# Kernel tuning notes

Hardware: AMD Instinct MI355X
Metric: run time of the kernel (lower is better)

## Reference

```python
import jax, jax.numpy as jnp
import numpy as np

BS, V, C, A = 8, 4096, 64, 12   # batch, vertices, channels, anchors (anchor_size=12 hardcoded in source)
K = 4                            # neighbor_num
POOLING_RATE = 4
POOL = V // POOLING_RATE


def setup_inputs() -> dict:
    key = jax.random.key(0)
    k1, k2, k3 = jax.random.split(key, 3)
    vertices = jax.random.normal(k1, (BS, V, 3), dtype=jnp.float32)
    feature_map = jax.random.normal(k2, (BS, C, V, A), dtype=jnp.float32)
    # deterministic stand-in for torch.randperm(V)[:POOL]
    sample_idx = jax.random.permutation(k3, V)[:POOL].astype(jnp.int32)
    return {"vertices": vertices, "feature_map": feature_map, "sample_idx": sample_idx}


def reference(vertices, feature_map, sample_idx):
    bs, v, _ = vertices.shape
    c, a = feature_map.shape[1], feature_map.shape[3]
    k = K
    # pairwise squared euclidean distances: (bs, v, v)
    inner = jnp.einsum('bic,bjc->bij', vertices, vertices)
    quad = jnp.sum(vertices * vertices, axis=2)                     # (bs, v)
    dist = -2.0 * inner + quad[:, None, :] + quad[:, :, None]
    # k+1 smallest, drop self (first entry)
    _, idx = jax.lax.top_k(-dist, k + 1)                            # (bs, v, k+1)
    nbr = idx[:, :, 1:]                                             # (bs, v, k)
    # gather neighbor features along vertex axis (axis=2 of feature_map)
    idx_b = jnp.broadcast_to(nbr.reshape(bs, 1, v * k, 1), (bs, c, v * k, a))
    nbr_feat = jnp.take_along_axis(feature_map, idx_b, axis=2)      # (bs, c, v*k, a)
    nbr_feat = nbr_feat.reshape(bs, c, v, k, a)
    pooled = jnp.max(nbr_feat, axis=3)                              # (bs, c, v, a)
    vertices_pool = vertices[:, sample_idx, :]                      # (bs, pool, 3)
    feature_map_pool = pooled[:, :, sample_idx, :]                  # (bs, c, pool, a)
    return vertices_pool, feature_map_pool
```

## Files before the change

### kernel.cpp

```cpp
#include <hip/hip_runtime.h>
#include <stdint.h>

#define BS 8
#define V 4096
#define C 64
#define A 12
#define POOL 1024

__device__ inline unsigned int ordu(float f) {
    unsigned int b = __float_as_uint(f);
    return b ^ ((unsigned int)(((int)b) >> 31) | 0x80000000u);
}
__device__ inline float unordu(unsigned int u) {
    unsigned int m = (~((unsigned int)(((int)u) >> 31))) | 0x80000000u;
    return __uint_as_float(u ^ m);
}

template<int NCC>
__global__ __launch_bounds__(256) void knn_chunk_kernel(
    const float* __restrict__ vtx,
    const int* __restrict__ sidx,
    unsigned long long* __restrict__ partial,
    unsigned int* __restrict__ counts)
{
    constexpr int CC = V / NCC;
    __shared__ float4 cand[CC];

    const int bid = blockIdx.x;
    const int tid = threadIdx.x;
    if (bid < (BS * V) / 256) counts[bid * 256 + tid] = 0;

    const int cc = bid % NCC;
    const int qc = (bid / NCC) & 3;
    const int b  = bid / (NCC * 4);

    const float* vb = vtx + (size_t)b * V * 3;

    for (int t = tid; t < CC; t += 256) {
        const int j = cc * CC + t;
        const float x = vb[j * 3 + 0];
        const float y = vb[j * 3 + 1];
        const float z = vb[j * 3 + 2];
        float q;
        {
#pragma clang fp contract(off)
            q = (x * x + y * y) + z * z;
        }
        cand[t] = make_float4(x, y, z, q);
    }
    __syncthreads();

    const int s = qc * 256 + tid;
    const int gq = sidx[s];
    const float qx = vb[gq * 3 + 0];
    const float qy = vb[gq * 3 + 1];
    const float qz = vb[gq * 3 + 2];
    float qq;
    {
#pragma clang fp contract(off)
        qq = (qx * qx + qy * qy) + qz * qz;
    }

    unsigned int h0 = ~0u, h1 = ~0u, h2 = ~0u, h3 = ~0u, h4 = ~0u;
    unsigned int l0 = 0, l1 = 0, l2 = 0, l3 = 0, l4 = 0;

#pragma unroll 8
    for (int jj = 0; jj < CC; ++jj) {
        const float4 cd = cand[jj];
        const float inner = fmaf(cd.z, qz, fmaf(cd.y, qy, cd.x * qx));
        const float d = fmaf(-2.0f, inner, cd.w) + qq;
        const unsigned int bits = __float_as_uint(d);
        const unsigned int u = bits ^ ((unsigned int)(((int)bits) >> 31) | 0x80000000u);
        const unsigned int idx = (unsigned int)(cc * CC + jj);
        if (u < h4) {
            const bool c0 = u < h0, c1 = u < h1, c2 = u < h2, c3 = u < h3;
            h4 = c3 ? h3 : u;              l4 = c3 ? l3 : idx;
            h3 = c3 ? (c2 ? h2 : u) : h3;  l3 = c3 ? (c2 ? l2 : idx) : l3;
            h2 = c2 ? (c1 ? h1 : u) : h2;  l2 = c2 ? (c1 ? l1 : idx) : l2;
            h1 = c1 ? (c0 ? h0 : u) : h1;  l1 = c1 ? (c0 ? l0 : idx) : l1;
            h0 = c0 ? u : h0;              l0 = c0 ? idx : l0;
        }
    }

    unsigned long long* p = partial + ((size_t)(b * POOL + s) * NCC + cc) * 5;
    p[0] = ((unsigned long long)h0 << 32) | l0;
    p[1] = ((unsigned long long)h1 << 32) | l1;
    p[2] = ((unsigned long long)h2 << 32) | l2;
    p[3] = ((unsigned long long)h3 << 32) | l3;
    p[4] = ((unsigned long long)h4 << 32) | l4;
}

template<int NCC>
__global__ __launch_bounds__(256) void knn_merge_kernel(
    const unsigned long long* __restrict__ partial,
    const float* __restrict__ vtx,
    const int* __restrict__ sidx,
    int* __restrict__ nbr,
    float* __restrict__ outv,
    unsigned int* __restrict__ counts)
{
    const int t = blockIdx.x * 256 + threadIdx.x;
    const int b = t / POOL;
    const int s = t % POOL;

    const unsigned long long* p = partial + (size_t)t * (NCC * 5);

    unsigned int h0 = ~0u, h1 = ~0u, h2 = ~0u, h3 = ~0u, h4 = ~0u;
    unsigned int l0 = 0, l1 = 0, l2 = 0, l3 = 0, l4 = 0;

#pragma unroll 4
    for (int ccc = 0; ccc < NCC; ++ccc) {
        const unsigned long long a0 = p[ccc * 5 + 0];
        const unsigned long long a1 = p[ccc * 5 + 1];
        const unsigned long long a2 = p[ccc * 5 + 2];
        const unsigned long long a3 = p[ccc * 5 + 3];
        const unsigned long long a4 = p[ccc * 5 + 4];
        if ((unsigned int)(a0 >> 32) < h4) {
#define INS(K)                                                               \
            {                                                                \
                const unsigned int u = (unsigned int)((K) >> 32);            \
                const unsigned int idx = (unsigned int)(K);                  \
                const bool c0 = u < h0, c1 = u < h1, c2 = u < h2,            \
                           c3 = u < h3, c4 = u < h4;                         \
                h4 = c4 ? (c3 ? h3 : u) : h4;                                \
                l4 = c4 ? (c3 ? l3 : idx) : l4;                              \
                h3 = c3 ? (c2 ? h2 : u) : h3;                                \
                l3 = c3 ? (c2 ? l2 : idx) : l3;                              \
                h2 = c2 ? (c1 ? h1 : u) : h2;                                \
                l2 = c2 ? (c1 ? l1 : idx) : l2;                              \
                h1 = c1 ? (c0 ? h0 : u) : h1;                                \
                l1 = c1 ? (c0 ? l0 : idx) : l1;                              \
                h0 = c0 ? u : h0;                                            \
                l0 = c0 ? idx : l0;                                          \
            }
            INS(a0) INS(a1) INS(a2) INS(a3) INS(a4)
#undef INS
        }
    }

    int4 nb;
    nb.x = (int)l1;
    nb.y = (int)l2;
    nb.z = (int)l3;
    nb.w = (int)l4;
    ((int4*)nbr)[t] = nb;

    unsigned int* cb = counts + b * V;
    atomicAdd(&cb[l1], 1u);
    atomicAdd(&cb[l2], 1u);
    atomicAdd(&cb[l3], 1u);
    atomicAdd(&cb[l4], 1u);

    const int gq = sidx[s];
    const float* vv = vtx + ((size_t)b * V + gq) * 3;
    outv[(size_t)t * 3 + 0] = vv[0];
    outv[(size_t)t * 3 + 1] = vv[1];
    outv[(size_t)t * 3 + 2] = vv[2];
}

__global__ __launch_bounds__(256) void scan_kernel(
    const unsigned int* __restrict__ counts,
    unsigned int* __restrict__ rowptr,
    unsigned int* __restrict__ cursors)
{
    const int b = blockIdx.x;
    const int tid = threadIdx.x;
    __shared__ unsigned int psum[256];

    const unsigned int* cb = counts + b * V;
    unsigned int local[16];
    unsigned int sum = 0;
#pragma unroll
    for (int i = 0; i < 16; ++i) { local[i] = sum; sum += cb[tid * 16 + i]; }
    psum[tid] = sum;
    __syncthreads();

    for (int off = 1; off < 256; off <<= 1) {
        unsigned int v = (tid >= off) ? psum[tid - off] : 0u;
        __syncthreads();
        psum[tid] += v;
        __syncthreads();
    }
    const unsigned int base = (tid == 0) ? 0u : psum[tid - 1];

    unsigned int* rp = rowptr + b * (V + 1);
    unsigned int* cu = cursors + b * V;
#pragma unroll
    for (int i = 0; i < 16; ++i) {
        const unsigned int e = base + local[i];
        rp[tid * 16 + i] = e;
        cu[tid * 16 + i] = e;
    }
    if (tid == 255) rp[V] = base + sum;
}

__global__ __launch_bounds__(256) void fill_kernel(
    const int* __restrict__ nbr,
    unsigned int* __restrict__ cursors,
    unsigned int* __restrict__ entries)
{
    const int t = blockIdx.x * 256 + threadIdx.x;
    const int b = t / POOL;
    const unsigned int s = (unsigned int)(t % POOL);
    const int4 nb = ((const int4*)nbr)[t];
    unsigned int* cu = cursors + b * V;
    unsigned int* en = entries + b * 4096;
    en[atomicAdd(&cu[nb.x], 1u)] = s;
    en[atomicAdd(&cu[nb.y], 1u)] = s;
    en[atomicAdd(&cu[nb.z], 1u)] = s;
    en[atomicAdd(&cu[nb.w], 1u)] = s;
}

__global__ __launch_bounds__(512) void pool_kernel(
    const float* __restrict__ fm,
    const unsigned int* __restrict__ rowptr,
    const unsigned int* __restrict__ entries,
    float* __restrict__ outf)
{
    __shared__ unsigned int pl[POOL * A];
    const int c = blockIdx.x % C;
    const int b = blockIdx.x / C;
    const int tid = threadIdx.x;

    {
        uint4* p4 = (uint4*)pl;
        const uint4 z = make_uint4(0u, 0u, 0u, 0u);
#pragma unroll
        for (int i = 0; i < 6; ++i) p4[tid + i * 512] = z;
    }
    __syncthreads();

    const unsigned int* rp = rowptr + b * (V + 1);
    const unsigned int* en = entries + b * 4096;
    const float4* plane = (const float4*)(fm + (size_t)(b * C + c) * V * A);

#pragma unroll 1
    for (int it = 0; it < V / 512; ++it) {
        const int j = it * 512 + tid;
        const unsigned int beg = rp[j];
        const unsigned int end = rp[j + 1];
        if (beg == end) continue;

        const float4 f0 = plane[j * 3 + 0];
        const float4 f1 = plane[j * 3 + 1];
        const float4 f2 = plane[j * 3 + 2];
        const unsigned int u0 = ordu(f0.x), u1 = ordu(f0.y), u2  = ordu(f0.z), u3  = ordu(f0.w);
        const unsigned int u4 = ordu(f1.x), u5 = ordu(f1.y), u6  = ordu(f1.z), u7  = ordu(f1.w);
        const unsigned int u8 = ordu(f2.x), u9 = ordu(f2.y), u10 = ordu(f2.z), u11 = ordu(f2.w);

        for (unsigned int e = beg; e < end; ++e) {
            unsigned int* d = pl + en[e] * A;
            atomicMax(d + 0, u0);  atomicMax(d + 1, u1);  atomicMax(d + 2, u2);
            atomicMax(d + 3, u3);  atomicMax(d + 4, u4);  atomicMax(d + 5, u5);
            atomicMax(d + 6, u6);  atomicMax(d + 7, u7);  atomicMax(d + 8, u8);
            atomicMax(d + 9, u9);  atomicMax(d + 10, u10); atomicMax(d + 11, u11);
        }
    }
    __syncthreads();

    const uint4* p4 = (const uint4*)pl;
    float4* dst = (float4*)(outf + (size_t)(b * C + c) * POOL * A);
#pragma unroll
    for (int i = 0; i < 6; ++i) {
        const uint4 v = p4[tid + i * 512];
        float4 f;
        f.x = unordu(v.x); f.y = unordu(v.y); f.z = unordu(v.z); f.w = unordu(v.w);
        dst[tid + i * 512] = f;
    }
}

extern "C" void kernel_launch(void* const* d_in, const int* in_sizes, int n_in,
                              void* d_out, int out_size, void* d_ws, size_t ws_size,
                              hipStream_t stream) {
    const float* vtx = (const float*)d_in[0];
    const float* fm  = (const float*)d_in[1];
    const int* sidx  = (const int*)d_in[2];
    float* out = (float*)d_out;

    float* outv = out;
    float* outf = out + (size_t)BS * POOL * 3;

    char* ws = (char*)d_ws;
    const size_t partial32_b = (size_t)BS * POOL * 32 * 5 * 8;
    const size_t partial16_b = (size_t)BS * POOL * 16 * 5 * 8;
    const size_t nbr_b     = (size_t)BS * POOL * 4 * 4;
    const size_t counts_b  = (size_t)BS * V * 4;
    const size_t rowptr_b  = (size_t)BS * (V + 1) * 4 + 28;
    const size_t cursors_b = (size_t)BS * V * 4;
    const size_t entries_b = (size_t)BS * 4096 * 4;
    const size_t tail_b = nbr_b + counts_b + rowptr_b + cursors_b + entries_b;

    const bool big = ws_size >= partial32_b + tail_b;
    const size_t partial_b = big ? partial32_b : partial16_b;

    unsigned long long* partial = (unsigned long long*)ws;
    int* nbr            = (int*)(ws + partial_b);
    unsigned int* counts  = (unsigned int*)(ws + partial_b + nbr_b);
    unsigned int* rowptr  = (unsigned int*)(ws + partial_b + nbr_b + counts_b);
    unsigned int* cursors = (unsigned int*)(ws + partial_b + nbr_b + counts_b + rowptr_b);
    unsigned int* entries = (unsigned int*)(ws + partial_b + nbr_b + counts_b + rowptr_b + cursors_b);

    if (big) {
        constexpr int NCC = 32;
        knn_chunk_kernel<NCC><<<BS * 4 * NCC, 256, 0, stream>>>(vtx, sidx, partial, counts);
        knn_merge_kernel<NCC><<<(BS * POOL) / 256, 256, 0, stream>>>(partial, vtx, sidx, nbr, outv, counts);
    } else {
        constexpr int NCC = 16;
        knn_chunk_kernel<NCC><<<BS * 4 * NCC, 256, 0, stream>>>(vtx, sidx, partial, counts);
        knn_merge_kernel<NCC><<<(BS * POOL) / 256, 256, 0, stream>>>(partial, vtx, sidx, nbr, outv, counts);
    }
    scan_kernel<<<BS, 256, 0, stream>>>(counts, rowptr, cursors);
    fill_kernel<<<(BS * POOL) / 256, 256, 0, stream>>>(nbr, cursors, entries);
    pool_kernel<<<BS * C, 512, 0, stream>>>(fm, rowptr, entries, outf);
}
```

Before: 229.1 us.

## Fuse scan and fill kernels, pad pooling LDS stride, compare floats in kNN

Merges the scan and fill kernels into one per-batch kernel that keeps the cursors in shared memory, which removes a launch and the global cursor array with its global atomics. The pool kernel pads each pooled row to a stride of 13 words in LDS to cut bank conflicts on the atomicMax scatter and the readback, at the cost of scalar LDS reads and more shared memory. The kNN chunk loop now compares float distances directly and converts them to ordered uints only at the final store. Fill parallelism drops to 8 blocks, and the LDS use per pool block grows.

```diff
diff --git a/kernel.cpp b/kernel.cpp
--- a/kernel.cpp
+++ b/kernel.cpp
@@ -6,6 +6,7 @@
 #define C 64
 #define A 12
 #define POOL 1024
+#define PSTRIDE 13
 
 __device__ inline unsigned int ordu(float f) {
     unsigned int b = __float_as_uint(f);
@@ -61,7 +62,8 @@
         qq = (qx * qx + qy * qy) + qz * qz;
     }
 
-    unsigned int h0 = ~0u, h1 = ~0u, h2 = ~0u, h3 = ~0u, h4 = ~0u;
+    const float INF = __uint_as_float(0x7F800000u);
+    float d0 = INF, d1 = INF, d2 = INF, d3 = INF, d4 = INF;
     unsigned int l0 = 0, l1 = 0, l2 = 0, l3 = 0, l4 = 0;
 
 #pragma unroll 8
@@ -69,25 +71,23 @@
         const float4 cd = cand[jj];
         const float inner = fmaf(cd.z, qz, fmaf(cd.y, qy, cd.x * qx));
         const float d = fmaf(-2.0f, inner, cd.w) + qq;
-        const unsigned int bits = __float_as_uint(d);
-        const unsigned int u = bits ^ ((unsigned int)(((int)bits) >> 31) | 0x80000000u);
         const unsigned int idx = (unsigned int)(cc * CC + jj);
-        if (u < h4) {
-            const bool c0 = u < h0, c1 = u < h1, c2 = u < h2, c3 = u < h3;
-            h4 = c3 ? h3 : u;              l4 = c3 ? l3 : idx;
-            h3 = c3 ? (c2 ? h2 : u) : h3;  l3 = c3 ? (c2 ? l2 : idx) : l3;
-            h2 = c2 ? (c1 ? h1 : u) : h2;  l2 = c2 ? (c1 ? l1 : idx) : l2;
-            h1 = c1 ? (c0 ? h0 : u) : h1;  l1 = c1 ? (c0 ? l0 : idx) : l1;
-            h0 = c0 ? u : h0;              l0 = c0 ? idx : l0;
+        if (d < d4) {
+            const bool c0 = d < d0, c1 = d < d1, c2 = d < d2, c3 = d < d3;
+            d4 = c3 ? d3 : d;              l4 = c3 ? l3 : idx;
+            d3 = c3 ? (c2 ? d2 : d) : d3;  l3 = c3 ? (c2 ? l2 : idx) : l3;
+            d2 = c2 ? (c1 ? d1 : d) : d2;  l2 = c2 ? (c1 ? l1 : idx) : l2;
+            d1 = c1 ? (c0 ? d0 : d) : d1;  l1 = c1 ? (c0 ? l0 : idx) : l1;
+            d0 = c0 ? d : d0;              l0 = c0 ? idx : l0;
         }
     }
 
     unsigned long long* p = partial + ((size_t)(b * POOL + s) * NCC + cc) * 5;
-    p[0] = ((unsigned long long)h0 << 32) | l0;
-    p[1] = ((unsigned long long)h1 << 32) | l1;
-    p[2] = ((unsigned long long)h2 << 32) | l2;
-    p[3] = ((unsigned long long)h3 << 32) | l3;
-    p[4] = ((unsigned long long)h4 << 32) | l4;
+    p[0] = ((unsigned long long)ordu(d0) << 32) | l0;
+    p[1] = ((unsigned long long)ordu(d1) << 32) | l1;
+    p[2] = ((unsigned long long)ordu(d2) << 32) | l2;
+    p[3] = ((unsigned long long)ordu(d3) << 32) | l3;
+    p[4] = ((unsigned long long)ordu(d4) << 32) | l4;
 }
 
 template<int NCC>
@@ -158,14 +158,16 @@
     outv[(size_t)t * 3 + 2] = vv[2];
 }
 
-__global__ __launch_bounds__(256) void scan_kernel(
+__global__ __launch_bounds__(256) void scan_fill_kernel(
     const unsigned int* __restrict__ counts,
+    const int* __restrict__ nbr,
     unsigned int* __restrict__ rowptr,
-    unsigned int* __restrict__ cursors)
+    unsigned int* __restrict__ entries)
 {
     const int b = blockIdx.x;
     const int tid = threadIdx.x;
     __shared__ unsigned int psum[256];
+    __shared__ unsigned int cur[V];
 
     const unsigned int* cb = counts + b * V;
     unsigned int local[16];
@@ -184,31 +186,25 @@
     const unsigned int base = (tid == 0) ? 0u : psum[tid - 1];
 
     unsigned int* rp = rowptr + b * (V + 1);
-    unsigned int* cu = cursors + b * V;
 #pragma unroll
     for (int i = 0; i < 16; ++i) {
         const unsigned int e = base + local[i];
         rp[tid * 16 + i] = e;
-        cu[tid * 16 + i] = e;
+        cur[tid * 16 + i] = e;
     }
     if (tid == 255) rp[V] = base + sum;
-}
-
-__global__ __launch_bounds__(256) void fill_kernel(
-    const int* __restrict__ nbr,
-    unsigned int* __restrict__ cursors,
-    unsigned int* __restrict__ entries)
-{
-    const int t = blockIdx.x * 256 + threadIdx.x;
-    const int b = t / POOL;
-    const unsigned int s = (unsigned int)(t % POOL);
-    const int4 nb = ((const int4*)nbr)[t];
-    unsigned int* cu = cursors + b * V;
+    __syncthreads();
+
     unsigned int* en = entries + b * 4096;
-    en[atomicAdd(&cu[nb.x], 1u)] = s;
-    en[atomicAdd(&cu[nb.y], 1u)] = s;
-    en[atomicAdd(&cu[nb.z], 1u)] = s;
-    en[atomicAdd(&cu[nb.w], 1u)] = s;
+#pragma unroll
+    for (int it = 0; it < POOL / 256; ++it) {
+        const int s = it * 256 + tid;
+        const int4 nb = ((const int4*)nbr)[b * POOL + s];
+        en[atomicAdd(&cur[nb.x], 1u)] = (unsigned int)s;
+        en[atomicAdd(&cur[nb.y], 1u)] = (unsigned int)s;
+        en[atomicAdd(&cur[nb.z], 1u)] = (unsigned int)s;
+        en[atomicAdd(&cur[nb.w], 1u)] = (unsigned int)s;
+    }
 }
 
 __global__ __launch_bounds__(512) void pool_kernel(
@@ -217,17 +213,12 @@
     const unsigned int* __restrict__ entries,
     float* __restrict__ outf)
 {
-    __shared__ unsigned int pl[POOL * A];
+    __shared__ unsigned int pl[POOL * PSTRIDE];
     const int c = blockIdx.x % C;
     const int b = blockIdx.x / C;
     const int tid = threadIdx.x;
 
-    {
-        uint4* p4 = (uint4*)pl;
-        const uint4 z = make_uint4(0u, 0u, 0u, 0u);
-#pragma unroll
-        for (int i = 0; i < 6; ++i) p4[tid + i * 512] = z;
-    }
+    for (int i = tid; i < POOL * PSTRIDE; i += 512) pl[i] = 0u;
     __syncthreads();
 
     const unsigned int* rp = rowptr + b * (V + 1);
@@ -249,7 +240,7 @@
         const unsigned int u8 = ordu(f2.x), u9 = ordu(f2.y), u10 = ordu(f2.z), u11 = ordu(f2.w);
 
         for (unsigned int e = beg; e < end; ++e) {
-            unsigned int* d = pl + en[e] * A;
+            unsigned int* d = pl + en[e] * PSTRIDE;
             atomicMax(d + 0, u0);  atomicMax(d + 1, u1);  atomicMax(d + 2, u2);
             atomicMax(d + 3, u3);  atomicMax(d + 4, u4);  atomicMax(d + 5, u5);
             atomicMax(d + 6, u6);  atomicMax(d + 7, u7);  atomicMax(d + 8, u8);
@@ -258,14 +249,17 @@
     }
     __syncthreads();
 
-    const uint4* p4 = (const uint4*)pl;
-    float4* dst = (float4*)(outf + (size_t)(b * C + c) * POOL * A);
+    float* dst = outf + (size_t)(b * C + c) * POOL * A;
 #pragma unroll
-    for (int i = 0; i < 6; ++i) {
-        const uint4 v = p4[tid + i * 512];
-        float4 f;
-        f.x = unordu(v.x); f.y = unordu(v.y); f.z = unordu(v.z); f.w = unordu(v.w);
-        dst[tid + i * 512] = f;
+    for (int it = 0; it < POOL / 512; ++it) {
+        const int s = it * 512 + tid;
+        const unsigned int* src = pl + s * PSTRIDE;
+        float4 o0, o1, o2;
+        o0.x = unordu(src[0]);  o0.y = unordu(src[1]);  o0.z = unordu(src[2]);  o0.w = unordu(src[3]);
+        o1.x = unordu(src[4]);  o1.y = unordu(src[5]);  o1.z = unordu(src[6]);  o1.w = unordu(src[7]);
+        o2.x = unordu(src[8]);  o2.y = unordu(src[9]);  o2.z = unordu(src[10]); o2.w = unordu(src[11]);
+        float4* d4 = (float4*)(dst + (size_t)s * A);
+        d4[0] = o0; d4[1] = o1; d4[2] = o2;
     }
 }
 
@@ -285,20 +279,18 @@
     const size_t partial16_b = (size_t)BS * POOL * 16 * 5 * 8;
     const size_t nbr_b     = (size_t)BS * POOL * 4 * 4;
     const size_t counts_b  = (size_t)BS * V * 4;
-    const size_t rowptr_b  = (size_t)BS * (V + 1) * 4 + 28;
-    const size_t cursors_b = (size_t)BS * V * 4;
+    const size_t rowptr_b  = (size_t)BS * (V + 1) * 4 + 32;
     const size_t entries_b = (size_t)BS * 4096 * 4;
-    const size_t tail_b = nbr_b + counts_b + rowptr_b + cursors_b + entries_b;
+    const size_t tail_b = nbr_b + counts_b + rowptr_b + entries_b;
 
     const bool big = ws_size >= partial32_b + tail_b;
     const size_t partial_b = big ? partial32_b : partial16_b;
 
     unsigned long long* partial = (unsigned long long*)ws;
-    int* nbr            = (int*)(ws + partial_b);
-    unsigned int* counts  = (unsigned int*)(ws + partial_b + nbr_b);
-    unsigned int* rowptr  = (unsigned int*)(ws + partial_b + nbr_b + counts_b);
-    unsigned int* cursors = (unsigned int*)(ws + partial_b + nbr_b + counts_b + rowptr_b);
-    unsigned int* entries = (unsigned int*)(ws + partial_b + nbr_b + counts_b + rowptr_b + cursors_b);
+    int* nbr             = (int*)(ws + partial_b);
+    unsigned int* counts = (unsigned int*)(ws + partial_b + nbr_b);
+    unsigned int* rowptr = (unsigned int*)(ws + partial_b + nbr_b + counts_b);
+    unsigned int* entries= (unsigned int*)(ws + partial_b + nbr_b + counts_b + rowptr_b);
 
     if (big) {
         constexpr int NCC = 32;
@@ -309,7 +301,6 @@
         knn_chunk_kernel<NCC><<<BS * 4 * NCC, 256, 0, stream>>>(vtx, sidx, partial, counts);
         knn_merge_kernel<NCC><<<(BS * POOL) / 256, 256, 0, stream>>>(partial, vtx, sidx, nbr, outv, counts);
     }
-    scan_kernel<<<BS, 256, 0, stream>>>(counts, rowptr, cursors);
-    fill_kernel<<<(BS * POOL) / 256, 256, 0, stream>>>(nbr, cursors, entries);
+    scan_fill_kernel<<<BS, 256, 0, stream>>>(counts, nbr, rowptr, entries);
     pool_kernel<<<BS * C, 512, 0, stream>>>(fm, rowptr, entries, outf);
 }
```

Measured after the change: 226.9 us. Within noise of the previous version (-1.0%).
